# Optimization experiments

Measured on AMD Instinct MI355X. Metric: run time of the kernel, lower is better.

Reference implementation:

```python
import jax, jax.numpy as jnp
import numpy as np

N = 100000      # nodes
E = 1_600_000   # edges (avg degree 16)
F = 128         # num_features
H = 128         # hidden
C = 10          # num_classes


def _agg_norm(row, col, mask, n, by_row):
    # A[dst=row, src=col]; scale rows (target) or cols (source) by mask,
    # remove any existing diagonal entries and add self-loops with value 1
    # (fill_diag(A,1.0)), then symmetric D^-1/2 A D^-1/2 normalization.
    m = mask[row] if by_row else mask[col]
    val = jnp.where(row == col, 0.0, m)              # off-diagonal edge values
    deg = jax.ops.segment_sum(val, row, num_segments=n) + 1.0  # +1 from self-loop
    dinv = deg ** -0.5                                # deg >= 1, never inf
    return dinv[row] * val * dinv[col], dinv * dinv   # edge vals, diag vals


def _spmm(val, diag, row, col, x, n):
    # y = A_hat @ x with off-diagonal edge list + explicit diagonal
    y = jax.ops.segment_sum(val[:, None] * x[col], row, num_segments=n)
    return y + diag[:, None] * x


def setup_inputs() -> dict:
    key = jax.random.key(0)
    ks = jax.random.split(key, 12)
    x = jax.random.normal(ks[0], (N, F), jnp.float32)
    src = jax.random.randint(ks[1], (E,), 0, N)
    dst = jax.random.randint(ks[2], (E,), 0, N)
    edge_index = jnp.stack([src, dst]).astype(jnp.int64)
    cc_mask = (jax.random.uniform(ks[3], (N,)) < 0.5).astype(jnp.float32)
    s = 0.05  # stand-in for xavier scale; exact init irrelevant to correctness
    W1L = jax.random.normal(ks[4], (F, H), jnp.float32) * s
    W1H = jax.random.normal(ks[5], (F, H), jnp.float32) * s
    W2L = jax.random.normal(ks[6], (H, H), jnp.float32) * s
    W2H = jax.random.normal(ks[7], (H, H), jnp.float32) * s
    WX = jax.random.normal(ks[8], (F, H), jnp.float32) * s
    lam1 = jnp.zeros((2,), jnp.float32)
    lam2 = jnp.zeros((2,), jnp.float32)
    lin_w = jax.random.normal(ks[9], (H, C), jnp.float32) * s
    lin_b = jnp.zeros((C,), jnp.float32)
    return {"x": x, "edge_index": edge_index, "cc_mask": cc_mask,
            "W1L": W1L, "W1H": W1H, "W2L": W2L, "W2H": W2H, "WX": WX,
            "lam1": lam1, "lam2": lam2, "lin_w": lin_w, "lin_b": lin_b}


def reference(x, edge_index, cc_mask, W1L, W1H, W2L, W2H, WX, lam1, lam2, lin_w, lin_b):
    n = x.shape[0]
    row = edge_index[1]   # destination (aggregation target)
    col = edge_index[0]   # source
    rev = 1.0 - cc_mask

    vl,  dl  = _agg_norm(row, col, cc_mask, n, True)    # target-masked (low)
    vll, dll = _agg_norm(row, col, cc_mask, n, False)   # source-masked (low)
    vh,  dh  = _agg_norm(row, col, rev,     n, True)    # target-masked (high)
    vhh, dhh = _agg_norm(row, col, rev,     n, False)   # source-masked (high)

    xl = jax.nn.relu(_spmm(vl, dl, row, col, x, n) @ W1L)
    xl = _spmm(vll, dll, row, col, xl, n) @ W2L

    xh = jax.nn.relu(_spmm(vh, dh, row, col, x, n) @ W1H)
    xh = _spmm(vhh, dhh, row, col, xh, n) @ W2H

    xc = x @ WX

    lamxl, laml = jax.nn.softmax(lam1)
    lamxh, lamh = jax.nn.softmax(lam2)
    lamx = lamxl * cc_mask + lamxh * rev                # per-node gate [N]

    xf = jax.nn.relu(lamx[:, None] * xc + laml * xl + lamh * xh)
    return xf @ lin_w + lin_b                           # [N, C] logits
```

## Files before the change

### kernel.cpp

```cpp
#include <hip/hip_runtime.h>
#include <stdint.h>

typedef unsigned int u32;
typedef unsigned short u16;
typedef unsigned long long u64;

#define DI __device__ __forceinline__

DI float bf2f(u16 u) { union { u32 i; float f; } v; v.i = ((u32)u) << 16; return v.f; }
DI u16 f2bf(float f) {
    union { u32 i; float f; } v; v.f = f;
    u32 u = v.i;
    u32 r = (u + 0x7fffu + ((u >> 16) & 1u)) >> 16;
    return (u16)r;
}
DI float2 unpack2(u32 x) { return make_float2(bf2f((u16)(x & 0xffffu)), bf2f((u16)(x >> 16))); }
DI u32 pack2(float a, float b) { return (u32)f2bf(a) | ((u32)f2bf(b) << 16); }

DI void fma8(float* acc, float w, uint4 xv) {
    float2 f0 = unpack2(xv.x), f1 = unpack2(xv.y), f2 = unpack2(xv.z), f3 = unpack2(xv.w);
    acc[0] += w * f0.x; acc[1] += w * f0.y; acc[2] += w * f1.x; acc[3] += w * f1.y;
    acc[4] += w * f2.x; acc[5] += w * f2.y; acc[6] += w * f3.x; acc[7] += w * f3.y;
}

DI uint4 scale8(uint4 v, float s) {
    uint4 r;
    float2 f;
    f = unpack2(v.x); r.x = pack2(f.x * s, f.y * s);
    f = unpack2(v.y); r.y = pack2(f.x * s, f.y * s);
    f = unpack2(v.z); r.z = pack2(f.x * s, f.y * s);
    f = unpack2(v.w); r.w = pack2(f.x * s, f.y * s);
    return r;
}


#define CHUNK 8192
#define NBPAD 800

__global__ __launch_bounds__(256) void head_k(const float* __restrict__ X, u16* __restrict__ Xb,
                                              int total4, int cvtBlocks, int maskBlocks,
                                              const float* __restrict__ mask, u64* __restrict__ bits, int n,
                                              const float* __restrict__ W1L, const float* __restrict__ W1H,
                                              const float* __restrict__ W2L, const float* __restrict__ W2H,
                                              const float* __restrict__ WX,
                                              const float* __restrict__ lam1, const float* __restrict__ lam2,
                                              u16* __restrict__ Bt,
                                              const int* __restrict__ ei, int E, int NB,
                                              u32* __restrict__ hist2d) {
    int bx = blockIdx.x;
    if (bx < cvtBlocks) {
        int i = bx * 256 + threadIdx.x;
        if (i >= total4) return;
        float4 v = ((const float4*)X)[i];
        ushort4 o;
        o.x = f2bf(v.x); o.y = f2bf(v.y); o.z = f2bf(v.z); o.w = f2bf(v.w);
        ((ushort4*)Xb)[i] = o;
        return;
    }
    bx -= cvtBlocks;
    if (bx < maskBlocks) {
        int i = bx * 256 + threadIdx.x;
        bool m = (i < n) && (mask[i] != 0.f);
        u64 word = __ballot(m);
        if ((threadIdx.x & 63) == 0 && i < n) bits[i >> 6] = word;
        return;
    }
    bx -= maskBlocks;
    if (bx < 320) {
        int w = bx >> 6;
        int idx = (bx & 63) * 256 + threadIdx.x;
        float scale = 1.f;
        if (w == 2) { float e0 = __expf(lam1[0]), e1 = __expf(lam1[1]); scale = e1 / (e0 + e1); }
        if (w == 3) { float f0 = __expf(lam2[0]), f1 = __expf(lam2[1]); scale = f1 / (f0 + f1); }
        const float* src = (w == 0) ? W1L : (w == 1) ? W1H : (w == 2) ? W2L : (w == 3) ? W2H : WX;
        int k = idx >> 7, nn = idx & 127;
        Bt[(size_t)w * 16384 + (size_t)nn * 128 + k] = f2bf(scale * src[idx]);
        return;
    }
    bx -= 320;
    __shared__ u32 hist[NBPAD];
    for (int i = threadIdx.x; i < NBPAD; i += 256) hist[i] = 0;
    __syncthreads();
    int base = bx * CHUNK;
    int end = min(base + CHUNK, E);
    for (int e = base + threadIdx.x; e < end; e += 256) {
        int c = ei[e], r = ei[E + e];
        if (r != c) atomicAdd(&hist[r >> 7], 1u);
    }
    __syncthreads();
    u32* out = hist2d + (size_t)bx * NBPAD;
    for (int i = threadIdx.x; i < NB; i += 256) out[i] = hist[i];
}

__global__ __launch_bounds__(256) void k_colscan(const u32* __restrict__ hist2d,
                                                 u32* __restrict__ off2d,
                                                 int NBLK, u32* __restrict__ btotal) {
    __shared__ u32 s[256];
    int t = blockIdx.x;
    int k = threadIdx.x;
    u32 v = (k < NBLK) ? hist2d[(size_t)k * NBPAD + t] : 0;
    s[k] = v;
    __syncthreads();
    for (int off = 1; off < 256; off <<= 1) {
        u32 tmp = (k >= off) ? s[k - off] : 0;
        __syncthreads();
        s[k] += tmp;
        __syncthreads();
    }
    if (k < NBLK) off2d[(size_t)k * NBPAD + t] = s[k] - v;
    if (k == 0) btotal[t] = s[255];
}

__global__ __launch_bounds__(1024) void k_basescan(const u32* __restrict__ btotal,
                                                   u32* __restrict__ bbase, int NB) {
    __shared__ u32 s[1024];
    int t = threadIdx.x;
    u32 v = (t < NB) ? btotal[t] : 0;
    s[t] = v;
    __syncthreads();
    for (int off = 1; off < 1024; off <<= 1) {
        u32 tmp = (t >= off) ? s[t - off] : 0;
        __syncthreads();
        s[t] += tmp;
        __syncthreads();
    }
    if (t < NB) bbase[t] = s[t] - v;
    if (t == NB - 1) bbase[NB] = s[t];
}

__global__ __launch_bounds__(256) void k_scatter(const int* __restrict__ ei, int E, int NB,
                                                 const u32* __restrict__ off2d,
                                                 const u32* __restrict__ bbase,
                                                 const u64* __restrict__ bits,
                                                 u32* __restrict__ bentry) {
    __shared__ u32 cur[NBPAD];
    const u32* off = off2d + (size_t)blockIdx.x * NBPAD;
    for (int i = threadIdx.x; i < NB; i += 256) cur[i] = off[i] + bbase[i];
    __syncthreads();
    int base = blockIdx.x * CHUNK;
    int end = min(base + CHUNK, E);
    for (int e = base + threadIdx.x; e < end; e += 256) {
        int c = ei[e], r = ei[E + e];
        if (r != c) {
            u32 pos = atomicAdd(&cur[r >> 7], 1u);
            u32 m = (u32)((bits[c >> 6] >> (c & 63)) & 1);
            bentry[pos] = (u32)(r & 127) | ((u32)c << 7) | (m << 31);
        }
    }
}

__global__ __launch_bounds__(256) void k_rowhist(const u32* __restrict__ bentry,
                                                 const u32* __restrict__ bbase,
                                                 u32* __restrict__ cntP, int n) {
    __shared__ u32 h[128];
    if (threadIdx.x < 128) h[threadIdx.x] = 0;
    __syncthreads();
    u32 s0 = bbase[blockIdx.x], s1 = bbase[blockIdx.x + 1];
    for (u32 i = s0 + threadIdx.x; i < s1; i += 256) {
        u32 e = bentry[i];
        atomicAdd(&h[e & 127], 1u + ((e >> 31) << 16));
    }
    __syncthreads();
    int row = blockIdx.x * 128 + threadIdx.x;
    if (threadIdx.x < 128 && row < n) cntP[row] = h[threadIdx.x];
}

#define SCAN_B 1024
__global__ __launch_bounds__(1024) void scanA(const u32* __restrict__ cntP, int* __restrict__ rowptr,
                                              int* __restrict__ blocksum, int n) {
    __shared__ int s[SCAN_B];
    int t = threadIdx.x;
    int i = blockIdx.x * SCAN_B + t;
    int v = (i < n) ? (int)(cntP[i] & 0xffffu) : 0;
    s[t] = v; __syncthreads();
    for (int off = 1; off < SCAN_B; off <<= 1) {
        int tmp = (t >= off) ? s[t - off] : 0;
        __syncthreads();
        s[t] += tmp;
        __syncthreads();
    }
    if (i < n) rowptr[i] = s[t] - v;
    if (t == SCAN_B - 1) blocksum[blockIdx.x] = s[t];
}

__global__ __launch_bounds__(256) void scanBC(const int* __restrict__ blocksum, int nblk,
                                              int* __restrict__ rowptr, const u32* __restrict__ cntP,
                                              const float* __restrict__ mask,
                                              int* __restrict__ mid,
                                              float* __restrict__ dinvL, float* __restrict__ dinvH,
                                              float* __restrict__ dinvLL, float* __restrict__ dinvHH,
                                              float2* __restrict__ diag1, float2* __restrict__ diag2, int n) {
    __shared__ int s[128];
    int t = threadIdx.x;
    if (t < 128) s[t] = (t < nblk) ? blocksum[t] : 0;
    __syncthreads();
    for (int off = 1; off < 128; off <<= 1) {
        int tmp = (t >= off && t < 128) ? s[t - off] : 0;
        __syncthreads();
        if (t < 128) s[t] += tmp;
        __syncthreads();
    }
    int blockoff = (blockIdx.x == 0) ? 0 : s[blockIdx.x - 1];
    if (blockIdx.x == 0 && t == 0) rowptr[n] = s[127];
#pragma unroll
    for (int k = 0; k < 4; k++) {
        int i = blockIdx.x * SCAN_B + k * 256 + t;
        if (i >= n) break;
        int v = rowptr[i] + blockoff;
        rowptr[i] = v;
        u32 p = cntP[i];
        int ci = (int)(p & 0xffffu);
        int cmi = (int)(p >> 16);
        mid[i] = v + cmi;
        float c = (float)ci;
        float cm = (float)cmi;
        bool mi = mask[i] != 0.f;
        float degL = (mi ? c : 0.f) + 1.f;
        float degH = (mi ? 0.f : c) + 1.f;
        float degLL = cm + 1.f;
        float degHH = (c - cm) + 1.f;
        dinvL[i] = rsqrtf(degL);
        dinvH[i] = rsqrtf(degH);
        dinvLL[i] = rsqrtf(degLL);
        dinvHH[i] = rsqrtf(degHH);
        diag1[i] = make_float2(1.f / degL, 1.f / degH);
        diag2[i] = make_float2(1.f / degLL, 1.f / degHH);
    }
}

__global__ __launch_bounds__(256) void k_place(const u32* __restrict__ bentry,
                                               const u32* __restrict__ bbase,
                                               const int* __restrict__ rowptr, const int* __restrict__ mid,
                                               int* __restrict__ sorted, int n) {
    __shared__ int cur[256];
    int row = blockIdx.x * 128 + threadIdx.x;
    if (threadIdx.x < 128) {
        int rr = min(row, n - 1);
        cur[threadIdx.x] = rowptr[rr];
        cur[128 + threadIdx.x] = mid[rr];
    }
    __syncthreads();
    u32 s0 = bbase[blockIdx.x], s1 = bbase[blockIdx.x + 1];
    for (u32 i = s0 + threadIdx.x; i < s1; i += 256) {
        u32 e = bentry[i];
        int rl = e & 127;
        int col = (int)((e >> 7) & 0x1FFFF);
        int isH = (int)((e >> 31) ^ 1u);
        int pos = atomicAdd(&cur[rl + (isH << 7)], 1);
        sorted[pos] = col;
    }
}


DI void gather_phase(const uint4* __restrict__ Xv, const int* __restrict__ sorted,
                     const float* __restrict__ dinv, float dr,
                     int e0, int e1, int q, int l16, float* acc) {
    int len = e1 - e0;
    int nfull = len >> 2;
    int e = e0;
#pragma unroll 2
    for (int it = 0; it < nfull; it++) {
        int c = sorted[e + q];
        float w = dr * dinv[c];
        uint4 xv = Xv[(size_t)c * 16 + l16];
        fma8(acc, w, xv);
        e += 4;
    }
    int rem = len & 3;
    if (rem) {
        int idx = min(e + q, e1 - 1);
        int c = sorted[idx];
        float w = (q < rem) ? dr * dinv[c] : 0.f;
        uint4 xv = Xv[(size_t)c * 16 + l16];
        fma8(acc, w, xv);
    }
}


__global__ __launch_bounds__(256) void spmm1(const u16* __restrict__ X,
                                             const int* __restrict__ rowptr, const int* __restrict__ sorted,
                                             const float* __restrict__ mask,
                                             const float* __restrict__ dinvL, const float* __restrict__ dinvH,
                                             const float2* __restrict__ diag1,
                                             u16* __restrict__ Yl, u16* __restrict__ Yh, int n) {
    int r = blockIdx.x * 4 + (threadIdx.x >> 6);
    if (r >= n) return;
    int lane = threadIdx.x & 63;
    int q = lane >> 4, l16 = lane & 15;
    bool mi = mask[r] != 0.f;
    const float* dinvA = mi ? dinvL : dinvH;
    float da = dinvA[r];
    float2 dg = diag1[r];
    float diag = mi ? dg.x : dg.y;

    const uint4* Xv = (const uint4*)X;
    uint4 xown = Xv[(size_t)r * 16 + l16];

    float acc[8] = {0.f, 0.f, 0.f, 0.f, 0.f, 0.f, 0.f, 0.f};
    int e0 = rowptr[r], e1 = rowptr[r + 1];
    gather_phase(Xv, sorted, dinvA, da, e0, e1, q, l16, acc);

#pragma unroll
    for (int k = 0; k < 8; k++) {
        acc[k] += __shfl_xor(acc[k], 16);
        acc[k] += __shfl_xor(acc[k], 32);
    }
    float2 o0 = unpack2(xown.x), o1 = unpack2(xown.y), o2 = unpack2(xown.z), o3 = unpack2(xown.w);
    uint4 res;
    res.x = pack2(acc[0] + diag * o0.x, acc[1] + diag * o0.y);
    res.y = pack2(acc[2] + diag * o1.x, acc[3] + diag * o1.y);
    res.z = pack2(acc[4] + diag * o2.x, acc[5] + diag * o2.y);
    res.w = pack2(acc[6] + diag * o3.x, acc[7] + diag * o3.y);
    uint4* Ya = (uint4*)(mi ? Yl : Yh);
    uint4* Yc = (uint4*)(mi ? Yh : Yl);
    if (q == 0) Ya[(size_t)r * 16 + l16] = res;
    if (q == 1) Yc[(size_t)r * 16 + l16] = xown;
}


__global__ __launch_bounds__(256) void spmm2(const u16* __restrict__ XL, const u16* __restrict__ XH,
                                             const int* __restrict__ rowptr, const int* __restrict__ mid,
                                             const int* __restrict__ sorted,
                                             const float* __restrict__ dinvLL, const float* __restrict__ dinvHH,
                                             const float2* __restrict__ diag2,
                                             u16* __restrict__ Zl, u16* __restrict__ Zh, int n) {
    int r = blockIdx.x * 4 + (threadIdx.x >> 6);
    if (r >= n) return;
    int lane = threadIdx.x & 63;
    int q = lane >> 4, l16 = lane & 15;

    float dllr = dinvLL[r], dhhr = dinvHH[r];
    float2 dg = diag2[r];

    const uint4* XLv = (const uint4*)XL;
    const uint4* XHv = (const uint4*)XH;
    uint4 xlown = XLv[(size_t)r * 16 + l16];
    uint4 xhown = XHv[(size_t)r * 16 + l16];

    float accL[8] = {0.f, 0.f, 0.f, 0.f, 0.f, 0.f, 0.f, 0.f};
    float accH[8] = {0.f, 0.f, 0.f, 0.f, 0.f, 0.f, 0.f, 0.f};
    int e0 = rowptr[r], m = mid[r], e1 = rowptr[r + 1];

    gather_phase(XLv, sorted, dinvLL, dllr, e0, m, q, l16, accL);
    gather_phase(XHv, sorted, dinvHH, dhhr, m, e1, q, l16, accH);

#pragma unroll
    for (int k = 0; k < 8; k++) {
        accL[k] += __shfl_xor(accL[k], 16);
        accL[k] += __shfl_xor(accL[k], 32);
        accH[k] += __shfl_xor(accH[k], 16);
        accH[k] += __shfl_xor(accH[k], 32);
    }
    float2 l0 = unpack2(xlown.x), l1 = unpack2(xlown.y), l2 = unpack2(xlown.z), l3 = unpack2(xlown.w);
    float2 h0 = unpack2(xhown.x), h1 = unpack2(xhown.y), h2 = unpack2(xhown.z), h3 = unpack2(xhown.w);
    float cl = dg.x, ch = dg.y;
    uint4 rl, rh;
    rl.x = pack2(accL[0] + cl * l0.x, accL[1] + cl * l0.y);
    rl.y = pack2(accL[2] + cl * l1.x, accL[3] + cl * l1.y);
    rl.z = pack2(accL[4] + cl * l2.x, accL[5] + cl * l2.y);
    rl.w = pack2(accL[6] + cl * l3.x, accL[7] + cl * l3.y);
    rh.x = pack2(accH[0] + ch * h0.x, accH[1] + ch * h0.y);
    rh.y = pack2(accH[2] + ch * h1.x, accH[3] + ch * h1.y);
    rh.z = pack2(accH[4] + ch * h2.x, accH[5] + ch * h2.y);
    rh.w = pack2(accH[6] + ch * h3.x, accH[7] + ch * h3.y);
    if (q == 0) ((uint4*)Zl)[(size_t)r * 16 + l16] = rl;
    if (q == 1) ((uint4*)Zh)[(size_t)r * 16 + l16] = rh;
}


typedef __attribute__((ext_vector_type(8))) short bf16x8;
typedef __attribute__((ext_vector_type(4))) float f32x4;

DI void stageB(const uint4* __restrict__ Bt4, uint4* Bs, int tid) {
#pragma unroll
    for (int i = 0; i < 8; i++) {
        int g = i * 256 + tid;
        int nn = g >> 4, c = g & 15;
        int d = ((nn >> 4) * 4 + (c >> 2)) * 64 + (c & 3) * 16 + (nn & 15);
        Bs[d] = Bt4[g];
    }
}

DI void loadA(uint4* a, const uint4* __restrict__ A4, int mr, int quad) {
#pragma unroll
    for (int kb = 0; kb < 4; kb++)
        a[kb] = A4[(size_t)mr * 16 + kb * 4 + quad];
}

DI void mfmaSec(const uint4* a, const uint4* Bs, f32x4* acc, int lane) {
#pragma unroll
    for (int nt = 0; nt < 8; nt++)
#pragma unroll
        for (int kb = 0; kb < 4; kb++) {
            bf16x8 av = *(const bf16x8*)&a[kb];
            bf16x8 bv = *(const bf16x8*)&Bs[(nt * 4 + kb) * 64 + lane];
            acc[nt] = __builtin_amdgcn_mfma_f32_16x16x32_bf16(av, bv, acc[nt], 0, 0, 0);
        }
}


__global__ __launch_bounds__(256) void gemm_lds(const u16* __restrict__ A0, const u16* __restrict__ Bt0,
                                                u16* __restrict__ C0,
                                                const u16* __restrict__ A1, const u16* __restrict__ Bt1,
                                                u16* __restrict__ C1, int M) {
    __shared__ uint4 Bs[2048];
    const u16* A = blockIdx.y ? A1 : A0;
    const u16* Bt = blockIdx.y ? Bt1 : Bt0;
    u16* C = blockIdx.y ? C1 : C0;

    int tid = threadIdx.x;
    int wave = tid >> 6, lane = tid & 63, quad = lane >> 4, l16 = lane & 15;
    int tile = blockIdx.x * 64;
    int m0 = tile + wave * 16 + l16;
    int mr = min(m0, M - 1);

    uint4 a[4];
    loadA(a, (const uint4*)A, mr, quad);
    stageB((const uint4*)Bt, Bs, tid);
    __syncthreads();

    f32x4 acc[8];
#pragma unroll
    for (int nt = 0; nt < 8; nt++) acc[nt] = f32x4{0.f, 0.f, 0.f, 0.f};
    mfmaSec(a, Bs, acc, lane);

    __syncthreads();
    u16* Cs = (u16*)Bs;
    int lrow0 = wave * 16 + quad * 4;
#pragma unroll
    for (int nt = 0; nt < 8; nt++)
#pragma unroll
        for (int rr = 0; rr < 4; rr++) {
            float v = acc[nt][rr];
            v = v > 0.f ? v : 0.f;
            Cs[(lrow0 + rr) * 128 + nt * 16 + l16] = f2bf(v);
        }
    __syncthreads();
    uint4* Cs4 = (uint4*)Bs;
    uint4* C4 = (uint4*)C;
#pragma unroll
    for (int i = 0; i < 4; i++) {
        int g = i * 256 + tid;
        int grow = tile + (g >> 4);
        if (grow < M) C4[(size_t)grow * 16 + (g & 15)] = Cs4[g];
    }
}


__global__ __launch_bounds__(256) void fused_final(const u16* __restrict__ Zl, const u16* __restrict__ Zh,
                                                   const u16* __restrict__ Xb,
                                                   const u16* __restrict__ BtL, const u16* __restrict__ BtH,
                                                   const u16* __restrict__ BtX,
                                                   const float* __restrict__ mask,
                                                   const float* __restrict__ lam1, const float* __restrict__ lam2,
                                                   const float* __restrict__ lin_w, const float* __restrict__ lin_b,
                                                   float* __restrict__ out, int M) {
    __shared__ uint4 Bs[2048];
    __shared__ float lws[1280];

    int tid = threadIdx.x;
    int wave = tid >> 6, lane = tid & 63, quad = lane >> 4, l16 = lane & 15;
    int tile = blockIdx.x * 64;
    int m0 = tile + wave * 16 + l16;
    int mr = min(m0, M - 1);

    uint4 a[4], an[4];
    loadA(a, (const uint4*)Zl, mr, quad);
    {
        const uint4* lw4 = (const uint4*)lin_w;
        uint4* lws4 = (uint4*)lws;
        lws4[tid] = lw4[tid];
        if (tid < 64) lws4[256 + tid] = lw4[256 + tid];
    }
    stageB((const uint4*)BtL, Bs, tid);

    float e0 = __expf(lam1[0]), e1 = __expf(lam1[1]);
    float lamxl = e0 / (e0 + e1);
    float f0 = __expf(lam2[0]), f1 = __expf(lam2[1]);
    float lamxh = f0 / (f0 + f1);
    float lamx = (mask[mr] != 0.f) ? lamxl : lamxh;

    __syncthreads();

    f32x4 acc[8];
#pragma unroll
    for (int nt = 0; nt < 8; nt++) acc[nt] = f32x4{0.f, 0.f, 0.f, 0.f};

    loadA(an, (const uint4*)Zh, mr, quad);
    mfmaSec(a, Bs, acc, lane);

    __syncthreads();
    stageB((const uint4*)BtH, Bs, tid);
#pragma unroll
    for (int kb = 0; kb < 4; kb++) a[kb] = an[kb];
    loadA(an, (const uint4*)Xb, mr, quad);
    __syncthreads();
    mfmaSec(a, Bs, acc, lane);

    __syncthreads();
    stageB((const uint4*)BtX, Bs, tid);
#pragma unroll
    for (int kb = 0; kb < 4; kb++) a[kb] = scale8(an[kb], lamx);
    __syncthreads();
    mfmaSec(a, Bs, acc, lane);

    int rbase = tile + wave * 16 + quad * 4;
    float part[4][10];
#pragma unroll
    for (int rr = 0; rr < 4; rr++)
#pragma unroll
        for (int c = 0; c < 10; c++) part[rr][c] = 0.f;

#pragma unroll
    for (int nt = 0; nt < 8; nt++) {
        const float* lw = lws + (nt * 16 + l16) * 10;
        float lwv[10];
#pragma unroll
        for (int c = 0; c < 10; c++) lwv[c] = lw[c];
#pragma unroll
        for (int rr = 0; rr < 4; rr++) {
            float p = acc[nt][rr];
            p = p > 0.f ? p : 0.f;
#pragma unroll
            for (int c = 0; c < 10; c++) part[rr][c] += p * lwv[c];
        }
    }
#pragma unroll
    for (int rr = 0; rr < 4; rr++)
#pragma unroll
        for (int c = 0; c < 10; c++) {
            part[rr][c] += __shfl_xor(part[rr][c], 1);
            part[rr][c] += __shfl_xor(part[rr][c], 2);
            part[rr][c] += __shfl_xor(part[rr][c], 4);
            part[rr][c] += __shfl_xor(part[rr][c], 8);
        }
    if (l16 == 0) {
#pragma unroll
        for (int rr = 0; rr < 4; rr++) {
            int row = rbase + rr;
            if (row < M) {
#pragma unroll
                for (int c = 0; c < 10; c++)
                    out[(size_t)row * 10 + c] = part[rr][c] + lin_b[c];
            }
        }
    }
}


extern "C" void kernel_launch(void* const* d_in, const int* in_sizes, int n_in,
                              void* d_out, int out_size, void* d_ws, size_t ws_size,
                              hipStream_t stream) {
    const float* x = (const float*)d_in[0];
    const int* ei = (const int*)d_in[1];
    const float* mask = (const float*)d_in[2];
    const float* W1L = (const float*)d_in[3];
    const float* W1H = (const float*)d_in[4];
    const float* W2L = (const float*)d_in[5];
    const float* W2H = (const float*)d_in[6];
    const float* WX = (const float*)d_in[7];
    const float* lam1 = (const float*)d_in[8];
    const float* lam2 = (const float*)d_in[9];
    const float* lin_w = (const float*)d_in[10];
    const float* lin_b = (const float*)d_in[11];
    float* out = (float*)d_out;

    int E = in_sizes[1] / 2;
    int n = in_sizes[2];
    int NB = (n + 127) >> 7;
    int NBLK = (E + CHUNK - 1) / CHUNK;

    char* w = (char*)d_ws;
    size_t off = 0;
    auto alloc = [&](size_t bytes) -> void* {
        off = (off + 255) & ~(size_t)255;
        void* p = w + off;
        off += bytes;
        return p;
    };
    u32* cntP = (u32*)alloc((size_t)n * 4);
    u64* bits = (u64*)alloc((size_t)((n + 63) / 64 + 1) * 8);
    int* rowptr = (int*)alloc((size_t)(n + 1) * 4);
    int* midp = (int*)alloc((size_t)n * 4);
    int* blocksum = (int*)alloc(128 * 4);
    u32* hist2d = (u32*)alloc((size_t)NBLK * NBPAD * 4);
    u32* off2d = (u32*)alloc((size_t)NBLK * NBPAD * 4);
    u32* btotal = (u32*)alloc((size_t)NBPAD * 4);
    u32* bbase = (u32*)alloc((size_t)(NB + 1) * 4);
    u32* bentry = (u32*)alloc((size_t)E * 4);
    int* sorted = (int*)alloc((size_t)E * 4);
    float* dinvL = (float*)alloc((size_t)n * 4);
    float* dinvH = (float*)alloc((size_t)n * 4);
    float* dinvLL = (float*)alloc((size_t)n * 4);
    float* dinvHH = (float*)alloc((size_t)n * 4);
    float2* diag1 = (float2*)alloc((size_t)n * 8);
    float2* diag2 = (float2*)alloc((size_t)n * 8);
    u16* Bt = (u16*)alloc(5 * 16384 * 2);
    size_t actb = (size_t)n * 128 * 2;
    u16* Xb = (u16*)alloc(actb);
    u16* B0 = (u16*)alloc(actb);
    u16* B1 = (u16*)alloc(actb);
    u16* B2 = (u16*)alloc(actb);
    u16* B3 = (u16*)alloc(actb);

    int nblkScan = (n + SCAN_B - 1) / SCAN_B;
    int total4 = n * 128 / 4;
    int cvtBlocks = (total4 + 255) / 256;
    int maskBlocks = ((n + 63) / 64 + 3) / 4;

    head_k<<<cvtBlocks + maskBlocks + 320 + NBLK, 256, 0, stream>>>(
        x, Xb, total4, cvtBlocks, maskBlocks, mask, bits, n,
        W1L, W1H, W2L, W2H, WX, lam1, lam2, Bt, ei, E, NB, hist2d);
    k_colscan<<<NB, 256, 0, stream>>>(hist2d, off2d, NBLK, btotal);
    k_basescan<<<1, 1024, 0, stream>>>(btotal, bbase, NB);
    k_scatter<<<NBLK, 256, 0, stream>>>(ei, E, NB, off2d, bbase, bits, bentry);
    k_rowhist<<<NB, 256, 0, stream>>>(bentry, bbase, cntP, n);
    scanA<<<nblkScan, 1024, 0, stream>>>(cntP, rowptr, blocksum, n);
    scanBC<<<nblkScan, 256, 0, stream>>>(blocksum, nblkScan, rowptr, cntP, mask, midp,
                                         dinvL, dinvH, dinvLL, dinvHH, diag1, diag2, n);
    k_place<<<NB, 256, 0, stream>>>(bentry, bbase, rowptr, midp, sorted, n);

    int rowsblk = (n + 3) / 4;
    int gemmblk = (n + 63) / 64;

    spmm1<<<rowsblk, 256, 0, stream>>>(Xb, rowptr, sorted, mask, dinvL, dinvH, diag1, B0, B1, n);
    gemm_lds<<<dim3(gemmblk, 2), 256, 0, stream>>>(B0, Bt + 0 * 16384, B2,
                                                   B1, Bt + 1 * 16384, B3, n);

    spmm2<<<rowsblk, 256, 0, stream>>>(B2, B3, rowptr, midp, sorted, dinvLL, dinvHH, diag2, B0, B1, n);

    fused_final<<<gemmblk, 256, 0, stream>>>(B0, B1, Xb,
                                             Bt + 2 * 16384, Bt + 3 * 16384, Bt + 4 * 16384,
                                             mask, lam1, lam2, lin_w, lin_b, out, n);
}
```

Before: 403.6 us.

## Precompute per-edge fp16 weights in placement and drop per-node dinv arrays

Edge-placement now computes per-edge normalization weights (source-side rsqrt factors) and stores them as fp16 arrays next to the sorted column indices. The SpMM kernels then read a contiguous weight stream instead of doing a random dinv[col] lookup per edge, and recompute the row-side factors from the counts. The spmm1 passthrough copy of unmasked rows is removed; the GEMM picks between the gathered buffer and the raw input based on the mask bit. Index math switches to 32-bit. This adds per-edge weight writes and fp16 rounding of the weights in exchange for fewer random gathers and fewer per-node arrays.

```diff
diff --git a/kernel.cpp b/kernel.cpp
--- a/kernel.cpp
+++ b/kernel.cpp
@@ -1,4 +1,5 @@
 #include <hip/hip_runtime.h>
+#include <hip/hip_fp16.h>
 #include <stdint.h>
 
 typedef unsigned int u32;
@@ -16,6 +17,9 @@
 }
 DI float2 unpack2(u32 x) { return make_float2(bf2f((u16)(x & 0xffffu)), bf2f((u16)(x >> 16))); }
 DI u32 pack2(float a, float b) { return (u32)f2bf(a) | ((u32)f2bf(b) << 16); }
+
+DI u16 f2h(float f) { __half h = __float2half_rn(f); return *(u16*)&h; }
+DI float h2f(u16 u) { __half h; *(u16*)&h = u; return __half2float(h); }
 
 DI void fma8(float* acc, float w, uint4 xv) {
     float2 f0 = unpack2(xv.x), f1 = unpack2(xv.y), f2 = unpack2(xv.z), f3 = unpack2(xv.w);
@@ -31,6 +35,10 @@
     f = unpack2(v.z); r.z = pack2(f.x * s, f.y * s);
     f = unpack2(v.w); r.w = pack2(f.x * s, f.y * s);
     return r;
+}
+
+DI int maskbit(const u64* __restrict__ bits, int i) {
+    return (int)((bits[i >> 6] >> (i & 63)) & 1);
 }
 
 
@@ -183,13 +191,8 @@
     if (t == SCAN_B - 1) blocksum[blockIdx.x] = s[t];
 }
 
-__global__ __launch_bounds__(256) void scanBC(const int* __restrict__ blocksum, int nblk,
-                                              int* __restrict__ rowptr, const u32* __restrict__ cntP,
-                                              const float* __restrict__ mask,
-                                              int* __restrict__ mid,
-                                              float* __restrict__ dinvL, float* __restrict__ dinvH,
-                                              float* __restrict__ dinvLL, float* __restrict__ dinvHH,
-                                              float2* __restrict__ diag1, float2* __restrict__ diag2, int n) {
+__global__ __launch_bounds__(256) void scanB2(const int* __restrict__ blocksum, int nblk,
+                                              int* __restrict__ rowptr, int n) {
     __shared__ int s[128];
     int t = threadIdx.x;
     if (t < 128) s[t] = (t < nblk) ? blocksum[t] : 0;
@@ -205,39 +208,24 @@
 #pragma unroll
     for (int k = 0; k < 4; k++) {
         int i = blockIdx.x * SCAN_B + k * 256 + t;
-        if (i >= n) break;
-        int v = rowptr[i] + blockoff;
-        rowptr[i] = v;
-        u32 p = cntP[i];
-        int ci = (int)(p & 0xffffu);
-        int cmi = (int)(p >> 16);
-        mid[i] = v + cmi;
-        float c = (float)ci;
-        float cm = (float)cmi;
-        bool mi = mask[i] != 0.f;
-        float degL = (mi ? c : 0.f) + 1.f;
-        float degH = (mi ? 0.f : c) + 1.f;
-        float degLL = cm + 1.f;
-        float degHH = (c - cm) + 1.f;
-        dinvL[i] = rsqrtf(degL);
-        dinvH[i] = rsqrtf(degH);
-        dinvLL[i] = rsqrtf(degLL);
-        dinvHH[i] = rsqrtf(degHH);
-        diag1[i] = make_float2(1.f / degL, 1.f / degH);
-        diag2[i] = make_float2(1.f / degLL, 1.f / degHH);
+        if (i < n) rowptr[i] += blockoff;
     }
 }
 
 __global__ __launch_bounds__(256) void k_place(const u32* __restrict__ bentry,
                                                const u32* __restrict__ bbase,
-                                               const int* __restrict__ rowptr, const int* __restrict__ mid,
-                                               int* __restrict__ sorted, int n) {
+                                               const int* __restrict__ rowptr,
+                                               const u32* __restrict__ cntP,
+                                               const u64* __restrict__ bits,
+                                               int* __restrict__ sorted,
+                                               u16* __restrict__ wgt1, u16* __restrict__ wgt2, int n) {
     __shared__ int cur[256];
     int row = blockIdx.x * 128 + threadIdx.x;
     if (threadIdx.x < 128) {
         int rr = min(row, n - 1);
-        cur[threadIdx.x] = rowptr[rr];
-        cur[128 + threadIdx.x] = mid[rr];
+        int rp = rowptr[rr];
+        cur[threadIdx.x] = rp;
+        cur[128 + threadIdx.x] = rp + (int)(cntP[rr] >> 16);
     }
     __syncthreads();
     u32 s0 = bbase[blockIdx.x], s1 = bbase[blockIdx.x + 1];
@@ -245,33 +233,42 @@
         u32 e = bentry[i];
         int rl = e & 127;
         int col = (int)((e >> 7) & 0x1FFFF);
-        int isH = (int)((e >> 31) ^ 1u);
+        u32 mc = e >> 31;
+        int isH = (int)(mc ^ 1u);
         int pos = atomicAdd(&cur[rl + (isH << 7)], 1);
+        int grow = blockIdx.x * 128 + rl;
+        u32 mr = (u32)((bits[grow >> 6] >> (grow & 63)) & 1);
+        u32 p = cntP[col];
+        float cnt = (float)(p & 0xffffu), cm = (float)(p >> 16);
+        float w1 = (mc == mr) ? rsqrtf(cnt + 1.f) : 1.f;
+        float w2 = mc ? rsqrtf(cm + 1.f) : rsqrtf(cnt - cm + 1.f);
         sorted[pos] = col;
-    }
-}
-
-
-DI void gather_phase(const uint4* __restrict__ Xv, const int* __restrict__ sorted,
-                     const float* __restrict__ dinv, float dr,
+        wgt1[pos] = f2h(w1);
+        wgt2[pos] = f2h(w2);
+    }
+}
+
+
+DI void gather_phase(const uint4* __restrict__ Xv, const int* __restrict__ cols,
+                     const u16* __restrict__ wgts,
                      int e0, int e1, int q, int l16, float* acc) {
     int len = e1 - e0;
     int nfull = len >> 2;
     int e = e0;
 #pragma unroll 2
     for (int it = 0; it < nfull; it++) {
-        int c = sorted[e + q];
-        float w = dr * dinv[c];
-        uint4 xv = Xv[(size_t)c * 16 + l16];
+        int c = cols[e + q];
+        float w = h2f(wgts[e + q]);
+        uint4 xv = Xv[(u32)(c * 16 + l16)];
         fma8(acc, w, xv);
         e += 4;
     }
     int rem = len & 3;
     if (rem) {
         int idx = min(e + q, e1 - 1);
-        int c = sorted[idx];
-        float w = (q < rem) ? dr * dinv[c] : 0.f;
-        uint4 xv = Xv[(size_t)c * 16 + l16];
+        int c = cols[idx];
+        float w = (q < rem) ? h2f(wgts[idx]) : 0.f;
+        uint4 xv = Xv[(u32)(c * 16 + l16)];
         fma8(acc, w, xv);
     }
 }
@@ -279,26 +276,24 @@
 
 __global__ __launch_bounds__(256) void spmm1(const u16* __restrict__ X,
                                              const int* __restrict__ rowptr, const int* __restrict__ sorted,
-                                             const float* __restrict__ mask,
-                                             const float* __restrict__ dinvL, const float* __restrict__ dinvH,
-                                             const float2* __restrict__ diag1,
+                                             const u16* __restrict__ wgt1,
+                                             const u64* __restrict__ bits, const u32* __restrict__ cntP,
                                              u16* __restrict__ Yl, u16* __restrict__ Yh, int n) {
     int r = blockIdx.x * 4 + (threadIdx.x >> 6);
     if (r >= n) return;
     int lane = threadIdx.x & 63;
     int q = lane >> 4, l16 = lane & 15;
-    bool mi = mask[r] != 0.f;
-    const float* dinvA = mi ? dinvL : dinvH;
-    float da = dinvA[r];
-    float2 dg = diag1[r];
-    float diag = mi ? dg.x : dg.y;
+    bool mi = maskbit(bits, r) != 0;
+    float cnt = (float)(cntP[r] & 0xffffu);
+    float da = rsqrtf(cnt + 1.f);
+    float diag = da * da;
 
     const uint4* Xv = (const uint4*)X;
-    uint4 xown = Xv[(size_t)r * 16 + l16];
+    uint4 xown = Xv[(u32)(r * 16 + l16)];
 
     float acc[8] = {0.f, 0.f, 0.f, 0.f, 0.f, 0.f, 0.f, 0.f};
     int e0 = rowptr[r], e1 = rowptr[r + 1];
-    gather_phase(Xv, sorted, dinvA, da, e0, e1, q, l16, acc);
+    gather_phase(Xv, sorted, wgt1, e0, e1, q, l16, acc);
 
 #pragma unroll
     for (int k = 0; k < 8; k++) {
@@ -307,42 +302,42 @@
     }
     float2 o0 = unpack2(xown.x), o1 = unpack2(xown.y), o2 = unpack2(xown.z), o3 = unpack2(xown.w);
     uint4 res;
-    res.x = pack2(acc[0] + diag * o0.x, acc[1] + diag * o0.y);
-    res.y = pack2(acc[2] + diag * o1.x, acc[3] + diag * o1.y);
-    res.z = pack2(acc[4] + diag * o2.x, acc[5] + diag * o2.y);
-    res.w = pack2(acc[6] + diag * o3.x, acc[7] + diag * o3.y);
+    res.x = pack2(da * acc[0] + diag * o0.x, da * acc[1] + diag * o0.y);
+    res.y = pack2(da * acc[2] + diag * o1.x, da * acc[3] + diag * o1.y);
+    res.z = pack2(da * acc[4] + diag * o2.x, da * acc[5] + diag * o2.y);
+    res.w = pack2(da * acc[6] + diag * o3.x, da * acc[7] + diag * o3.y);
     uint4* Ya = (uint4*)(mi ? Yl : Yh);
-    uint4* Yc = (uint4*)(mi ? Yh : Yl);
-    if (q == 0) Ya[(size_t)r * 16 + l16] = res;
-    if (q == 1) Yc[(size_t)r * 16 + l16] = xown;
+    if (q == 0) Ya[(u32)(r * 16 + l16)] = res;
 }
 
 
 __global__ __launch_bounds__(256) void spmm2(const u16* __restrict__ XL, const u16* __restrict__ XH,
-                                             const int* __restrict__ rowptr, const int* __restrict__ mid,
-                                             const int* __restrict__ sorted,
-                                             const float* __restrict__ dinvLL, const float* __restrict__ dinvHH,
-                                             const float2* __restrict__ diag2,
+                                             const int* __restrict__ rowptr, const int* __restrict__ sorted,
+                                             const u16* __restrict__ wgt2, const u32* __restrict__ cntP,
                                              u16* __restrict__ Zl, u16* __restrict__ Zh, int n) {
     int r = blockIdx.x * 4 + (threadIdx.x >> 6);
     if (r >= n) return;
     int lane = threadIdx.x & 63;
     int q = lane >> 4, l16 = lane & 15;
 
-    float dllr = dinvLL[r], dhhr = dinvHH[r];
-    float2 dg = diag2[r];
+    u32 p = cntP[r];
+    float cnt = (float)(p & 0xffffu), cm = (float)(p >> 16);
+    float dllr = rsqrtf(cm + 1.f);
+    float dhhr = rsqrtf(cnt - cm + 1.f);
+    float cl = dllr * dllr, ch = dhhr * dhhr;
+    int e0 = rowptr[r], e1 = rowptr[r + 1];
+    int m = e0 + (int)(p >> 16);
 
     const uint4* XLv = (const uint4*)XL;
     const uint4* XHv = (const uint4*)XH;
-    uint4 xlown = XLv[(size_t)r * 16 + l16];
-    uint4 xhown = XHv[(size_t)r * 16 + l16];
+    uint4 xlown = XLv[(u32)(r * 16 + l16)];
+    uint4 xhown = XHv[(u32)(r * 16 + l16)];
 
     float accL[8] = {0.f, 0.f, 0.f, 0.f, 0.f, 0.f, 0.f, 0.f};
     float accH[8] = {0.f, 0.f, 0.f, 0.f, 0.f, 0.f, 0.f, 0.f};
-    int e0 = rowptr[r], m = mid[r], e1 = rowptr[r + 1];
-
-    gather_phase(XLv, sorted, dinvLL, dllr, e0, m, q, l16, accL);
-    gather_phase(XHv, sorted, dinvHH, dhhr, m, e1, q, l16, accH);
+
+    gather_phase(XLv, sorted, wgt2, e0, m, q, l16, accL);
+    gather_phase(XHv, sorted, wgt2, m, e1, q, l16, accH);
 
 #pragma unroll
     for (int k = 0; k < 8; k++) {
@@ -353,18 +348,17 @@
     }
     float2 l0 = unpack2(xlown.x), l1 = unpack2(xlown.y), l2 = unpack2(xlown.z), l3 = unpack2(xlown.w);
     float2 h0 = unpack2(xhown.x), h1 = unpack2(xhown.y), h2 = unpack2(xhown.z), h3 = unpack2(xhown.w);
-    float cl = dg.x, ch = dg.y;
     uint4 rl, rh;
-    rl.x = pack2(accL[0] + cl * l0.x, accL[1] + cl * l0.y);
-    rl.y = pack2(accL[2] + cl * l1.x, accL[3] + cl * l1.y);
-    rl.z = pack2(accL[4] + cl * l2.x, accL[5] + cl * l2.y);
-    rl.w = pack2(accL[6] + cl * l3.x, accL[7] + cl * l3.y);
-    rh.x = pack2(accH[0] + ch * h0.x, accH[1] + ch * h0.y);
-    rh.y = pack2(accH[2] + ch * h1.x, accH[3] + ch * h1.y);
-    rh.z = pack2(accH[4] + ch * h2.x, accH[5] + ch * h2.y);
-    rh.w = pack2(accH[6] + ch * h3.x, accH[7] + ch * h3.y);
-    if (q == 0) ((uint4*)Zl)[(size_t)r * 16 + l16] = rl;
-    if (q == 1) ((uint4*)Zh)[(size_t)r * 16 + l16] = rh;
+    rl.x = pack2(dllr * accL[0] + cl * l0.x, dllr * accL[1] + cl * l0.y);
+    rl.y = pack2(dllr * accL[2] + cl * l1.x, dllr * accL[3] + cl * l1.y);
+    rl.z = pack2(dllr * accL[4] + cl * l2.x, dllr * accL[5] + cl * l2.y);
+    rl.w = pack2(dllr * accL[6] + cl * l3.x, dllr * accL[7] + cl * l3.y);
+    rh.x = pack2(dhhr * accH[0] + ch * h0.x, dhhr * accH[1] + ch * h0.y);
+    rh.y = pack2(dhhr * accH[2] + ch * h1.x, dhhr * accH[3] + ch * h1.y);
+    rh.z = pack2(dhhr * accH[4] + ch * h2.x, dhhr * accH[5] + ch * h2.y);
+    rh.w = pack2(dhhr * accH[6] + ch * h3.x, dhhr * accH[7] + ch * h3.y);
+    if (q == 0) ((uint4*)Zl)[(u32)(r * 16 + l16)] = rl;
+    if (q == 1) ((uint4*)Zh)[(u32)(r * 16 + l16)] = rh;
 }
 
 
@@ -402,11 +396,14 @@
 __global__ __launch_bounds__(256) void gemm_lds(const u16* __restrict__ A0, const u16* __restrict__ Bt0,
                                                 u16* __restrict__ C0,
                                                 const u16* __restrict__ A1, const u16* __restrict__ Bt1,
-                                                u16* __restrict__ C1, int M) {
+                                                u16* __restrict__ C1,
+                                                const u16* __restrict__ Xb, const u64* __restrict__ bits,
+                                                int M) {
     __shared__ uint4 Bs[2048];
-    const u16* A = blockIdx.y ? A1 : A0;
-    const u16* Bt = blockIdx.y ? Bt1 : Bt0;
-    u16* C = blockIdx.y ? C1 : C0;
+    int job = blockIdx.y;
+    const u16* A = job ? A1 : A0;
+    const u16* Bt = job ? Bt1 : Bt0;
+    u16* C = job ? C1 : C0;
 
     int tid = threadIdx.x;
     int wave = tid >> 6, lane = tid & 63, quad = lane >> 4, l16 = lane & 15;
@@ -414,8 +411,12 @@
     int m0 = tile + wave * 16 + l16;
     int mr = min(m0, M - 1);
 
+    int mi = maskbit(bits, mr);
+    bool useGathered = job ? (mi == 0) : (mi != 0);
+    const uint4* src = useGathered ? (const uint4*)A : (const uint4*)Xb;
+
     uint4 a[4];
-    loadA(a, (const uint4*)A, mr, quad);
+    loadA(a, src, mr, quad);
     stageB((const uint4*)Bt, Bs, tid);
     __syncthreads();
 
@@ -581,7 +582,6 @@
     u32* cntP = (u32*)alloc((size_t)n * 4);
     u64* bits = (u64*)alloc((size_t)((n + 63) / 64 + 1) * 8);
     int* rowptr = (int*)alloc((size_t)(n + 1) * 4);
-    int* midp = (int*)alloc((size_t)n * 4);
     int* blocksum = (int*)alloc(128 * 4);
     u32* hist2d = (u32*)alloc((size_t)NBLK * NBPAD * 4);
     u32* off2d = (u32*)alloc((size_t)NBLK * NBPAD * 4);
@@ -589,12 +589,8 @@
     u32* bbase = (u32*)alloc((size_t)(NB + 1) * 4);
     u32* bentry = (u32*)alloc((size_t)E * 4);
     int* sorted = (int*)alloc((size_t)E * 4);
-    float* dinvL = (float*)alloc((size_t)n * 4);
-    float* dinvH = (float*)alloc((size_t)n * 4);
-    float* dinvLL = (float*)alloc((size_t)n * 4);
-    float* dinvHH = (float*)alloc((size_t)n * 4);
-    float2* diag1 = (float2*)alloc((size_t)n * 8);
-    float2* diag2 = (float2*)alloc((size_t)n * 8);
+    u16* wgt1 = (u16*)alloc((size_t)E * 2);
+    u16* wgt2 = (u16*)alloc((size_t)E * 2);
     u16* Bt = (u16*)alloc(5 * 16384 * 2);
     size_t actb = (size_t)n * 128 * 2;
     u16* Xb = (u16*)alloc(actb);
@@ -616,18 +612,17 @@
     k_scatter<<<NBLK, 256, 0, stream>>>(ei, E, NB, off2d, bbase, bits, bentry);
     k_rowhist<<<NB, 256, 0, stream>>>(bentry, bbase, cntP, n);
     scanA<<<nblkScan, 1024, 0, stream>>>(cntP, rowptr, blocksum, n);
-    scanBC<<<nblkScan, 256, 0, stream>>>(blocksum, nblkScan, rowptr, cntP, mask, midp,
-                                         dinvL, dinvH, dinvLL, dinvHH, diag1, diag2, n);
-    k_place<<<NB, 256, 0, stream>>>(bentry, bbase, rowptr, midp, sorted, n);
+    scanB2<<<nblkScan, 256, 0, stream>>>(blocksum, nblkScan, rowptr, n);
+    k_place<<<NB, 256, 0, stream>>>(bentry, bbase, rowptr, cntP, bits, sorted, wgt1, wgt2, n);
 
     int rowsblk = (n + 3) / 4;
     int gemmblk = (n + 63) / 64;
 
-    spmm1<<<rowsblk, 256, 0, stream>>>(Xb, rowptr, sorted, mask, dinvL, dinvH, diag1, B0, B1, n);
+    spmm1<<<rowsblk, 256, 0, stream>>>(Xb, rowptr, sorted, wgt1, bits, cntP, B0, B1, n);
     gemm_lds<<<dim3(gemmblk, 2), 256, 0, stream>>>(B0, Bt + 0 * 16384, B2,
-                                                   B1, Bt + 1 * 16384, B3, n);
-
-    spmm2<<<rowsblk, 256, 0, stream>>>(B2, B3, rowptr, midp, sorted, dinvLL, dinvHH, diag2, B0, B1, n);
+                                                   B1, Bt + 1 * 16384, B3, Xb, bits, n);
+
+    spmm2<<<rowsblk, 256, 0, stream>>>(B2, B3, rowptr, sorted, wgt2, cntP, B0, B1, n);
 
     fused_final<<<gemmblk, 256, 0, stream>>>(B0, B1, Xb,
                                              Bt + 2 * 16384, Bt + 3 * 16384, Bt + 4 * 16384,
```

Result: no change. 401.5 us (-0.5%).
